# Kernel optimization log

Hardware: AMD Instinct MI355X
Metric: run time of the kernel (lower is better)

Reference implementation:

```python
import jax, jax.numpy as jnp
import numpy as np
from jax import lax

EPS = 1e-5

def conv2d(x, w, b, pad):
    # x: [N,C,H,W], w: [O,I,kh,kw]
    y = lax.conv_general_dilated(x, w, (1, 1), [(pad, pad), (pad, pad)],
                                 dimension_numbers=('NCHW', 'OIHW', 'NCHW'))
    return y + b[None, :, None, None]

def bn(x, g, b, axes, pshape):
    # training-mode batch norm (biased variance), matching torch BatchNorm2d in train()
    m = jnp.mean(x, axes, keepdims=True)
    v = jnp.var(x, axes, keepdims=True)
    return (x - m) * lax.rsqrt(v + EPS) * g.reshape(pshape) + b.reshape(pshape)

def maxpool2(x):
    return lax.reduce_window(x, -jnp.inf, lax.max, (1, 1, 2, 2), (1, 1, 2, 2), 'VALID')

def setup_inputs() -> dict:
    key = jax.random.key(0)
    ks = jax.random.split(key, 8)
    B, S, C, H, W = 8, 20, 16, 96, 96
    inp = {
        'anchor': jax.random.normal(ks[0], (B, C, H, W), jnp.float32),
        'support': jax.random.normal(ks[1], (B, S, C, H, W), jnp.float32),
        'cw': jax.random.normal(ks[2], (16, 16, 3, 3), jnp.float32) * 0.1,
        'cb': jnp.zeros((16,), jnp.float32),
        'cg': jnp.ones((16,), jnp.float32),
        'cbt': jnp.zeros((16,), jnp.float32),
        'pw': jax.random.normal(ks[3], (16, 32, 1, 1), jnp.float32) * 0.1,
        'pb': jnp.zeros((16,), jnp.float32),
        'pg': jnp.ones((16,), jnp.float32),
        'pbt': jnp.zeros((16,), jnp.float32),
        'jw': jax.random.normal(ks[4], (16, 16, 3, 3), jnp.float32) * 0.1,
        'jb': jnp.zeros((16,), jnp.float32),
        'jg': jnp.ones((16,), jnp.float32),
        'jbt': jnp.zeros((16,), jnp.float32),
        'rw': jax.random.normal(ks[5], (16, 16, 3, 3), jnp.float32) * 0.1,
        'rb': jnp.zeros((16,), jnp.float32),
        'rg': jnp.ones((16,), jnp.float32),
        'rbt': jnp.zeros((16,), jnp.float32),
    }
    return inp

def reference(anchor, support, cw, cb, cg, cbt, pw, pb, pg, pbt,
              jw, jb, jg, jbt, rw, rb, rg, rbt):
    B, S, C, H, W = support.shape
    # reshaper(anchor): conv3x3 -> BN -> ReLU -> maxpool2   (BN stats over B,H,W)
    ax = maxpool2(jax.nn.relu(bn(conv2d(anchor, rw, rb, 1), rg, rbt, (0, 2, 3), (1, -1, 1, 1))))
    # reshaper(support flattened): BN stats pooled over B*S,H,W (matches torch view(-1,...))
    sflat = support.reshape(B * S, C, H, W)
    sr = maxpool2(jax.nn.relu(bn(conv2d(sflat, rw, rb, 1), rg, rbt, (0, 2, 3), (1, -1, 1, 1))))
    sr = sr.reshape(B, S, C, H // 2, W // 2)
    # concentrator(support flattened)
    sx = jax.nn.relu(bn(conv2d(sflat, cw, cb, 1), cg, cbt, (0, 2, 3), (1, -1, 1, 1)))
    sx = sx.reshape(B, S, C, H, W)
    # leave-one-out sum via total-sum trick (O(S) instead of O(S^2))
    loo = sx.sum(axis=1, keepdims=True) - sx              # [B,S,C,H,W]
    cat = jnp.concatenate([support, loo], axis=2)         # [B,S,2C,H,W]
    pe = conv2d(cat.reshape(B * S, 2 * C, H, W), pw, pb, 0).reshape(B, S, C, H, W)
    # torch loop applies perm_equi per-i: BN stats over (B,H,W) for each support index
    pe = jax.nn.relu(bn(pe, pg, pbt, (0, 3, 4), (1, 1, -1, 1, 1)))
    deep = pe.mean(axis=1)                                # [B,C,H,W]
    # projector: conv3x3 -> BN -> softmax over channels -> maxpool2
    proj = maxpool2(jax.nn.softmax(bn(conv2d(deep, jw, jb, 1), jg, jbt, (0, 2, 3), (1, -1, 1, 1)), axis=1))
    anchor_out = ax * proj                                # [B,C,H/2,W/2]
    support_out = sr * proj[:, None]                      # [B,S,C,H/2,W/2]
    return anchor_out, support_out
```

## Files before the change

### kernel.cpp

```cpp
#include <hip/hip_runtime.h>
#include <stdint.h>

#define EPS_BN 1e-5f

typedef __attribute__((ext_vector_type(8))) short short8;
typedef __attribute__((ext_vector_type(4))) float floatx4;

__device__ __forceinline__ unsigned short f2bf(float f) {
    unsigned u = __builtin_bit_cast(unsigned, f);
    u += 0x7fffu + ((u >> 16) & 1u);
    return (unsigned short)(u >> 16);
}
__device__ __forceinline__ float bf2f(unsigned short h) {
    unsigned u = ((unsigned)h) << 16;
    return __builtin_bit_cast(float, u);
}
__device__ __forceinline__ void unpack8(uint4 q, float* v) {
    v[0] = bf2f((unsigned short)q.x); v[1] = bf2f((unsigned short)(q.x >> 16));
    v[2] = bf2f((unsigned short)q.y); v[3] = bf2f((unsigned short)(q.y >> 16));
    v[4] = bf2f((unsigned short)q.z); v[5] = bf2f((unsigned short)(q.z >> 16));
    v[6] = bf2f((unsigned short)q.w); v[7] = bf2f((unsigned short)(q.w >> 16));
}
__device__ __forceinline__ uint4 pack8(const float* v) {
    uint4 q;
    q.x = (unsigned)f2bf(v[0]) | ((unsigned)f2bf(v[1]) << 16);
    q.y = (unsigned)f2bf(v[2]) | ((unsigned)f2bf(v[3]) << 16);
    q.z = (unsigned)f2bf(v[4]) | ((unsigned)f2bf(v[5]) << 16);
    q.w = (unsigned)f2bf(v[6]) | ((unsigned)f2bf(v[7]) << 16);
    return q;
}

__device__ __forceinline__ void async_copy16(const unsigned short* g, unsigned short* l) {
    __builtin_amdgcn_global_load_lds(
        (const __attribute__((address_space(1))) unsigned int*)(const void*)g,
        (__attribute__((address_space(3))) unsigned int*)(void*)l,
        16, 0, 0);
}

__device__ __forceinline__ void bn_coef(const float* st, int n, int c, float invN,
                                        const float* gg, const float* bb,
                                        float* scl, float* shf) {
    const float mean = st[c] * invN;
    const float var = st[n + c] * invN - mean * mean;
    const float sc = gg[c & 15] * rsqrtf(var + EPS_BN);
    scl[c] = sc;
    shf[c] = bb[c & 15] - mean * sc;
}

__global__ __launch_bounds__(256)
void pack_kernel(const float* __restrict__ support, const float* __restrict__ anchor,
                 unsigned short* __restrict__ spad, unsigned short* __restrict__ apad,
                 const float* __restrict__ rw, const float* __restrict__ cw,
                 const float* __restrict__ jw, unsigned short* __restrict__ frag,
                 float* __restrict__ stats)
{
    const int tid = threadIdx.x;
    if (blockIdx.x >= 6303) {
        const int bx = blockIdx.x - 6303;
        if (bx == 4) {
            #pragma unroll
            for (int k = 0; k < 3; ++k) stats[k * 256 + tid] = 0.f;
            return;
        }
        const int idx = bx * 256 + tid;
        if (idx >= 960) return;
        const int combo = idx >> 6, lane = idx & 63;
        const int cv = combo / 5, j = combo - cv * 5;
        const float* w = (cv == 0) ? rw : (cv == 1) ? cw : jw;
        const int o = lane & 15, g = lane >> 4;
        unsigned short e8[8];
        #pragma unroll
        for (int e = 0; e < 8; ++e) {
            const int k = j * 32 + g * 8 + e;
            unsigned short val = 0;
            if (k < 144) {
                const int t = k >> 4, i = k & 15;
                const int kh = t / 3, kw = t - kh * 3;
                val = f2bf(w[((o * 16 + i) * 3 + kh) * 3 + kw]);
            }
            e8[e] = val;
        }
        *(uint4*)(frag + ((size_t)combo * 64 + lane) * 8) =
            make_uint4((unsigned)e8[0] | ((unsigned)e8[1] << 16), (unsigned)e8[2] | ((unsigned)e8[3] << 16),
                       (unsigned)e8[4] | ((unsigned)e8[5] << 16), (unsigned)e8[6] | ((unsigned)e8[7] << 16));
        return;
    }
    const int idx = blockIdx.x * 256 + tid;
    if (idx >= 168 * 9604) return;
    const int img = idx / 9604;
    const int rem = idx - img * 9604;
    const int pr = rem / 98, pc = rem - pr * 98;
    const int gh = pr - 1, gw = pc - 1;
    const bool ok = (gh >= 0) & (gh < 96) & (gw >= 0) & (gw < 96);
    const float* src = (img < 160) ? (support + (size_t)img * 147456)
                                   : (anchor + (size_t)(img - 160) * 147456);
    unsigned short* dst = (img < 160) ? (spad + (size_t)img * 9604 * 16)
                                      : (apad + (size_t)(img - 160) * 9604 * 16);
    const int gbase = gh * 96 + gw;
    unsigned pk[8];
    #pragma unroll
    for (int c = 0; c < 8; ++c) {
        const float v0 = ok ? src[(2 * c) * 9216 + gbase] : 0.f;
        const float v1 = ok ? src[(2 * c + 1) * 9216 + gbase] : 0.f;
        pk[c] = (unsigned)f2bf(v0) | ((unsigned)f2bf(v1) << 16);
    }
    const int sw = (pc >> 2) & 1;
    unsigned short* p = dst + (size_t)rem * 16;
    *(uint4*)(p + (sw << 3)) = make_uint4(pk[0], pk[1], pk[2], pk[3]);
    *(uint4*)(p + ((sw ^ 1) << 3)) = make_uint4(pk[4], pk[5], pk[6], pk[7]);
}

template<bool POOLA>
__device__ __forceinline__ void conv_tile(
    unsigned short* lds, float* red,
    const unsigned short* __restrict__ imgin,
    const unsigned short* __restrict__ fragA, const float* __restrict__ bA,
    const unsigned short* __restrict__ fragB, const float* __restrict__ bB,
    unsigned short* __restrict__ outAimg, unsigned short* __restrict__ outBimg,
    float* __restrict__ statsA, float* __restrict__ statsB,
    const int r0b, const bool two)
{
    const int tid = threadIdx.x;
    const int lane = tid & 63;
    const int wv = tid >> 6;

    const unsigned short* gsrc = imgin + (size_t)(r0b * 8 * 98) * 16;
    #pragma unroll
    for (int k = 0; k < 8; ++k) {
        const int chunk = k * 256 + tid;
        if (chunk < 1960)
            async_copy16(gsrc + (size_t)chunk * 8, lds + (k * 256 + wv * 64) * 8);
    }

    const int n = lane & 15, g = lane >> 4;
    short8 fA[5], fB[5];
    #pragma unroll
    for (int j = 0; j < 5; ++j) {
        fA[j] = *(const short8*)(fragA + ((size_t)j * 64 + lane) * 8);
        if (two) fB[j] = *(const short8*)(fragB + ((size_t)j * 64 + lane) * 8);
    }
    const float4 bA4 = *(const float4*)(bA + 4 * g);
    float4 bB4 = make_float4(0.f, 0.f, 0.f, 0.f);
    if (two) bB4 = *(const float4*)(bB + 4 * g);
    const float biasA[4] = {bA4.x, bA4.y, bA4.z, bA4.w};
    const float biasB[4] = {bB4.x, bB4.y, bB4.z, bB4.w};

    __syncthreads();

    float s1A[4] = {0.f, 0.f, 0.f, 0.f}, s2A[4] = {0.f, 0.f, 0.f, 0.f};
    float s1B[4] = {0.f, 0.f, 0.f, 0.f}, s2B[4] = {0.f, 0.f, 0.f, 0.f};

    for (int cg = 0; cg < 6; ++cg) {
        float pA[2][4], pB[2][4];
        #pragma unroll
        for (int tr = 0; tr < 2; ++tr) {
            const int lr = 2 * wv + tr;
            floatx4 aA = {0.f, 0.f, 0.f, 0.f};
            floatx4 aB = {0.f, 0.f, 0.f, 0.f};
            #pragma unroll
            for (int j = 0; j < 5; ++j) {
                const int t = (j < 4) ? (2 * j + (g >> 1)) : 8;
                const int kh = t / 3, kw = t - kh * 3;
                const int ldscol = cg * 16 + n + kw;
                const int half = (g & 1) ^ ((ldscol >> 2) & 1);
                const short8 a = *(const short8*)&lds[((lr + kh) * 98 + ldscol) * 16 + (half << 3)];
                aA = __builtin_amdgcn_mfma_f32_16x16x32_bf16(fA[j], a, aA, 0, 0, 0);
                if (two) aB = __builtin_amdgcn_mfma_f32_16x16x32_bf16(fB[j], a, aB, 0, 0, 0);
            }
            #pragma unroll
            for (int r = 0; r < 4; ++r) {
                const float vA = aA[r] + biasA[r];
                pA[tr][r] = vA; s1A[r] += vA; s2A[r] += vA * vA;
                if (two) {
                    const float vB = aB[r] + biasB[r];
                    pB[tr][r] = vB; s1B[r] += vB; s2B[r] += vB * vB;
                }
            }
            const int grow = r0b * 8 + lr;
            const size_t pixbase = ((size_t)(grow * 96 + cg * 16 + n)) * 16 + 4 * g;
            if (two)
                *(uint2*)(outBimg + pixbase) =
                    make_uint2((unsigned)f2bf(pB[tr][0]) | ((unsigned)f2bf(pB[tr][1]) << 16),
                               (unsigned)f2bf(pB[tr][2]) | ((unsigned)f2bf(pB[tr][3]) << 16));
            if (!POOLA)
                *(uint2*)(outAimg + pixbase) =
                    make_uint2((unsigned)f2bf(pA[tr][0]) | ((unsigned)f2bf(pA[tr][1]) << 16),
                               (unsigned)f2bf(pA[tr][2]) | ((unsigned)f2bf(pA[tr][3]) << 16));
        }
        if (POOLA) {
            float pm[4];
            #pragma unroll
            for (int r = 0; r < 4; ++r) {
                pm[r] = fmaxf(pA[0][r], pA[1][r]);
                pm[r] = fmaxf(pm[r], __shfl_xor(pm[r], 1));
            }
            if (!(n & 1)) {
                const int orow = r0b * 4 + wv;
                const size_t ob = ((size_t)(orow * 48 + cg * 8 + (n >> 1))) * 16 + 4 * g;
                *(uint2*)(outAimg + ob) =
                    make_uint2((unsigned)f2bf(pm[0]) | ((unsigned)f2bf(pm[1]) << 16),
                               (unsigned)f2bf(pm[2]) | ((unsigned)f2bf(pm[3]) << 16));
            }
        }
    }

    #pragma unroll
    for (int r = 0; r < 4; ++r) {
        #pragma unroll
        for (int d = 1; d < 16; d <<= 1) {
            s1A[r] += __shfl_xor(s1A[r], d); s2A[r] += __shfl_xor(s2A[r], d);
            if (two) { s1B[r] += __shfl_xor(s1B[r], d); s2B[r] += __shfl_xor(s2B[r], d); }
        }
    }
    if (n == 0) {
        #pragma unroll
        for (int r = 0; r < 4; ++r) {
            red[(wv * 4 + 0) * 16 + g * 4 + r] = s1A[r];
            red[(wv * 4 + 1) * 16 + g * 4 + r] = s2A[r];
            if (two) {
                red[(wv * 4 + 2) * 16 + g * 4 + r] = s1B[r];
                red[(wv * 4 + 3) * 16 + g * 4 + r] = s2B[r];
            }
        }
    }
    __syncthreads();
    if (tid < (two ? 64 : 32)) {
        const int st = tid >> 4, oc = tid & 15;
        const float v = red[(0 * 4 + st) * 16 + oc] + red[(1 * 4 + st) * 16 + oc] +
                        red[(2 * 4 + st) * 16 + oc] + red[(3 * 4 + st) * 16 + oc];
        float* dst = (st < 2) ? statsA : statsB;
        atomicAdd(&dst[(st & 1) * 16 + oc], v);
    }
}

__global__ __launch_bounds__(256)
void conv_main_kernel(const unsigned short* __restrict__ spad, const unsigned short* __restrict__ apad,
                      const unsigned short* __restrict__ fragR, const float* __restrict__ rb,
                      const unsigned short* __restrict__ fragC, const float* __restrict__ cb,
                      unsigned short* __restrict__ srp, unsigned short* __restrict__ sxpe,
                      unsigned short* __restrict__ axp,
                      float* __restrict__ statsSr, float* __restrict__ statsSx,
                      float* __restrict__ statsAx)
{
    __shared__ __align__(16) unsigned short lds[10 * 98 * 16];
    __shared__ float red[4 * 4 * 16];
    const bool two = blockIdx.x < 1920;
    const int bid = two ? blockIdx.x : blockIdx.x - 1920;
    const int img = bid / 12;
    const int r0b = bid - img * 12;
    const unsigned short* in = (two ? spad : apad) + (size_t)img * 9604 * 16;
    unsigned short* outA = (two ? srp : axp) + (size_t)img * 2304 * 16;
    unsigned short* outB = sxpe + (size_t)img * 9216 * 16;
    conv_tile<true>(lds, red, in, fragR, rb, fragC, cb, outA, outB,
                    two ? statsSr : statsAx, statsSx, r0b, two);
}

__global__ __launch_bounds__(256)
void conv_j_kernel(const unsigned short* __restrict__ deeppad,
                   const unsigned short* __restrict__ fragJ, const float* __restrict__ jb,
                   unsigned short* __restrict__ pre_j, float* __restrict__ statsJ)
{
    __shared__ __align__(16) unsigned short lds[10 * 98 * 16];
    __shared__ float red[4 * 4 * 16];
    const int img = blockIdx.x / 12;
    const int r0b = blockIdx.x - img * 12;
    conv_tile<false>(lds, red, deeppad + (size_t)img * 9604 * 16, fragJ, jb, nullptr, nullptr,
                     pre_j + (size_t)img * 9216 * 16, nullptr, statsJ, nullptr, r0b, false);
}

__global__ __launch_bounds__(256)
void sxsum_kernel(const unsigned short* __restrict__ sx, const float* __restrict__ statsSx,
                  const float* __restrict__ cgm, const float* __restrict__ cbt,
                  float* __restrict__ out, unsigned short* __restrict__ deeppad)
{
    __shared__ float scl[16], shf[16];
    __shared__ float part[3][64][17];
    const int tid = threadIdx.x;
    if (blockIdx.x < 13) {
        const int idx = blockIdx.x * 256 + tid;
        if (idx < 8 * 388) {
            const int img = idx / 388;
            const int h = idx - img * 388;
            int pr, pc;
            if (h < 98)       { pr = 0;           pc = h; }
            else if (h < 196) { pr = 97;          pc = h - 98; }
            else if (h < 292) { pr = h - 196 + 1; pc = 0; }
            else              { pr = h - 292 + 1; pc = 97; }
            unsigned short* p = deeppad + ((size_t)img * 9604 + pr * 98 + pc) * 16;
            *(uint4*)p = make_uint4(0, 0, 0, 0);
            *(uint4*)(p + 8) = make_uint4(0, 0, 0, 0);
        }
    }
    if (tid < 16) bn_coef(statsSx, 16, tid, 1.f / 1474560.f, cgm, cbt, scl, shf);
    const int b = blockIdx.x / 144;
    const int chunk = blockIdx.x - b * 144;
    const int px = tid & 63, sg = tid >> 6;
    const int pix = chunk * 64 + px;
    __syncthreads();
    float acc[16];
    #pragma unroll
    for (int c = 0; c < 16; ++c) acc[c] = 0.f;
    const unsigned short* p = sx + ((size_t)(b * 20 + sg * 5) * 9216 + pix) * 16;
    #pragma unroll
    for (int s = 0; s < 5; ++s) {
        float v[16];
        unpack8(*(const uint4*)p, v);
        unpack8(*(const uint4*)(p + 8), v + 8);
        #pragma unroll
        for (int c = 0; c < 16; ++c) acc[c] += fmaxf(v[c] * scl[c] + shf[c], 0.f);
        p += 9216 * 16;
    }
    if (sg > 0) {
        #pragma unroll
        for (int c = 0; c < 16; ++c) part[sg - 1][px][c] = acc[c];
    }
    __syncthreads();
    if (sg == 0) {
        #pragma unroll
        for (int c = 0; c < 16; ++c) acc[c] += part[0][px][c] + part[1][px][c] + part[2][px][c];
        float* o = out + ((size_t)b * 9216 + pix) * 16;
        #pragma unroll
        for (int q = 0; q < 4; ++q)
            *(float4*)(o + 4 * q) = make_float4(acc[4 * q], acc[4 * q + 1], acc[4 * q + 2], acc[4 * q + 3]);
    }
}

__global__ __launch_bounds__(256)
void pe_kernel(const unsigned short* __restrict__ spad, unsigned short* __restrict__ sxpe,
               const float* __restrict__ sxsum, const float* __restrict__ statsSx,
               const float* __restrict__ cgm, const float* __restrict__ cbt,
               const float* __restrict__ pw, const float* __restrict__ pb,
               float* __restrict__ statsPe)
{
    __shared__ float sscl[16], sshf[16];
    __shared__ float red[4][2][16];
    const int tid = threadIdx.x;
    if (tid < 16) bn_coef(statsSx, 16, tid, 1.f / 1474560.f, cgm, cbt, sscl, sshf);
    const int lane = tid & 63, wv = tid >> 6;
    const int p = lane & 15, g = lane >> 4;
    const int img = blockIdx.x / 9;
    const int chunk = blockIdx.x - img * 9;
    const int b = img / 20, s = img - b * 20;
    const int c0 = (g & 1) * 8;

    short8 fw;
    {
        const float4 wa = *(const float4*)(pw + p * 32 + g * 8);
        const float4 wb = *(const float4*)(pw + p * 32 + g * 8 + 4);
        fw[0] = (short)f2bf(wa.x); fw[1] = (short)f2bf(wa.y);
        fw[2] = (short)f2bf(wa.z); fw[3] = (short)f2bf(wa.w);
        fw[4] = (short)f2bf(wb.x); fw[5] = (short)f2bf(wb.y);
        fw[6] = (short)f2bf(wb.z); fw[7] = (short)f2bf(wb.w);
    }
    const float4 b4 = *(const float4*)(pb + 4 * g);
    const float bias[4] = {b4.x, b4.y, b4.z, b4.w};
    __syncthreads();
    float scl[8], shf[8];
    #pragma unroll
    for (int e = 0; e < 8; ++e) { scl[e] = sscl[c0 + e]; shf[e] = sshf[c0 + e]; }

    const unsigned short* imgspad = spad + (size_t)img * 9604 * 16;
    unsigned short* imgsx = sxpe + (size_t)img * 9216 * 16;
    const float* bsum = sxsum + (size_t)b * 9216 * 16;

    float s1[4] = {0.f, 0.f, 0.f, 0.f}, s2[4] = {0.f, 0.f, 0.f, 0.f};

    for (int it = 0; it < 16; ++it) {
        const int pix = chunk * 1024 + it * 64 + wv * 16 + p;
        short8 bf;
        if (g < 2) {
            const int row = pix / 96, col = pix - row * 96;
            const int sw = ((col + 1) >> 2) & 1;
            bf = *(const short8*)(imgspad + ((row + 1) * 98 + col + 1) * 16 + (((g ^ sw) & 1) << 3));
        } else {
            float xv[8];
            unpack8(*(const uint4*)(imgsx + (size_t)pix * 16 + c0), xv);
            const float* sm = bsum + (size_t)pix * 16 + c0;
            const float4 sma = *(const float4*)sm;
            const float4 smb = *(const float4*)(sm + 4);
            const float smv[8] = {sma.x, sma.y, sma.z, sma.w, smb.x, smb.y, smb.z, smb.w};
            #pragma unroll
            for (int e = 0; e < 8; ++e) {
                const float loo = smv[e] - fmaxf(xv[e] * scl[e] + shf[e], 0.f);
                bf[e] = (short)f2bf(loo);
            }
        }
        floatx4 acc = {0.f, 0.f, 0.f, 0.f};
        acc = __builtin_amdgcn_mfma_f32_16x16x32_bf16(fw, bf, acc, 0, 0, 0);
        const float v0 = acc[0] + bias[0], v1 = acc[1] + bias[1];
        const float v2 = acc[2] + bias[2], v3 = acc[3] + bias[3];
        s1[0] += v0; s1[1] += v1; s1[2] += v2; s1[3] += v3;
        s2[0] += v0 * v0; s2[1] += v1 * v1; s2[2] += v2 * v2; s2[3] += v3 * v3;
        *(uint2*)(imgsx + (size_t)pix * 16 + 4 * g) =
            make_uint2((unsigned)f2bf(v0) | ((unsigned)f2bf(v1) << 16),
                       (unsigned)f2bf(v2) | ((unsigned)f2bf(v3) << 16));
    }

    #pragma unroll
    for (int r = 0; r < 4; ++r) {
        #pragma unroll
        for (int d = 1; d < 16; d <<= 1) {
            s1[r] += __shfl_xor(s1[r], d);
            s2[r] += __shfl_xor(s2[r], d);
        }
    }
    if (p == 0) {
        #pragma unroll
        for (int r = 0; r < 4; ++r) { red[wv][0][g * 4 + r] = s1[r]; red[wv][1][g * 4 + r] = s2[r]; }
    }
    __syncthreads();
    if (tid < 32) {
        const int st = tid >> 4, c = tid & 15;
        const float v = red[0][st][c] + red[1][st][c] + red[2][st][c] + red[3][st][c];
        atomicAdd(&statsPe[st * 320 + s * 16 + c], v);
    }
}

__global__ __launch_bounds__(256)
void deep_kernel(const unsigned short* __restrict__ pe, const float* __restrict__ statsPe,
                 const float* __restrict__ pg, const float* __restrict__ pbt,
                 unsigned short* __restrict__ deeppad)
{
    __shared__ float scl[320], shf[320];
    __shared__ float part[3][64][17];
    const int tid = threadIdx.x;
    for (int i = tid; i < 320; i += 256)
        bn_coef(statsPe, 320, i, 1.f / 73728.f, pg, pbt, scl, shf);
    const int b = blockIdx.x / 144;
    const int chunk = blockIdx.x - b * 144;
    const int px = tid & 63, sg = tid >> 6;
    const int pix = chunk * 64 + px;
    __syncthreads();
    float acc[16];
    #pragma unroll
    for (int c = 0; c < 16; ++c) acc[c] = 0.f;
    const unsigned short* p = pe + ((size_t)(b * 20 + sg * 5) * 9216 + pix) * 16;
    #pragma unroll
    for (int s = 0; s < 5; ++s) {
        const int si = sg * 5 + s;
        float v[16];
        unpack8(*(const uint4*)p, v);
        unpack8(*(const uint4*)(p + 8), v + 8);
        #pragma unroll
        for (int c = 0; c < 16; ++c) acc[c] += fmaxf(v[c] * scl[si * 16 + c] + shf[si * 16 + c], 0.f);
        p += 9216 * 16;
    }
    if (sg > 0) {
        #pragma unroll
        for (int c = 0; c < 16; ++c) part[sg - 1][px][c] = acc[c];
    }
    __syncthreads();
    if (sg == 0) {
        #pragma unroll
        for (int c = 0; c < 16; ++c)
            acc[c] = (acc[c] + part[0][px][c] + part[1][px][c] + part[2][px][c]) * 0.05f;
        const int row = pix / 96, col = pix - row * 96;
        const int sw = ((col + 1) >> 2) & 1;
        unsigned short* d = deeppad + ((size_t)b * 9604 + (row + 1) * 98 + col + 1) * 16;
        *(uint4*)(d + (sw << 3)) = pack8(acc);
        *(uint4*)(d + ((sw ^ 1) << 3)) = pack8(acc + 8);
    }
}

__global__ __launch_bounds__(256)
void proj_kernel(const unsigned short* __restrict__ pj, const float* __restrict__ statsJ,
                 const float* __restrict__ jg, const float* __restrict__ jbt,
                 float* __restrict__ proj)
{
    __shared__ float scl[16], shf[16];
    const int tid = threadIdx.x;
    if (tid < 16) bn_coef(statsJ, 16, tid, 1.f / 73728.f, jg, jbt, scl, shf);
    const int b = blockIdx.x / 9;
    const int opix = (blockIdx.x - b * 9) * 256 + tid;
    __syncthreads();
    const int oi = opix / 48, oj = opix - oi * 48;
    float mx[16];
    #pragma unroll
    for (int c = 0; c < 16; ++c) mx[c] = 0.f;
    #pragma unroll
    for (int dy = 0; dy < 2; ++dy) {
        const unsigned short* q = pj + ((size_t)b * 9216 + (2 * oi + dy) * 96 + 2 * oj) * 16;
        #pragma unroll
        for (int dx = 0; dx < 2; ++dx) {
            float v[16]; float mval = -1e30f;
            unpack8(*(const uint4*)(q + dx * 16), v);
            unpack8(*(const uint4*)(q + dx * 16 + 8), v + 8);
            #pragma unroll
            for (int c = 0; c < 16; ++c) { v[c] = v[c] * scl[c] + shf[c]; mval = fmaxf(mval, v[c]); }
            float ssum = 0.f;
            #pragma unroll
            for (int c = 0; c < 16; ++c) { v[c] = __expf(v[c] - mval); ssum += v[c]; }
            const float inv = 1.f / ssum;
            #pragma unroll
            for (int c = 0; c < 16; ++c) mx[c] = fmaxf(mx[c], v[c] * inv);
        }
    }
    float* o = proj + ((size_t)b * 2304 + opix) * 16;
    #pragma unroll
    for (int q2 = 0; q2 < 4; ++q2)
        *(float4*)(o + 4 * q2) = make_float4(mx[4 * q2], mx[4 * q2 + 1], mx[4 * q2 + 2], mx[4 * q2 + 3]);
}

__global__ __launch_bounds__(256)
void out_kernel(const unsigned short* __restrict__ srp, const unsigned short* __restrict__ axp,
                const float* __restrict__ statsSr, const float* __restrict__ statsAx,
                const float* __restrict__ rg, const float* __restrict__ rbt,
                const float* __restrict__ proj, float* __restrict__ outS,
                float* __restrict__ outA)
{
    __shared__ float scl[16], shf[16];
    const int tid = threadIdx.x;
    const bool sup = blockIdx.x < 1440;
    if (tid < 16) {
        if (sup) bn_coef(statsSr, 16, tid, 1.f / 1474560.f, rg, rbt, scl, shf);
        else     bn_coef(statsAx, 16, tid, 1.f / 73728.f, rg, rbt, scl, shf);
    }
    const int bid = sup ? blockIdx.x : blockIdx.x - 1440;
    const int bs = bid / 9;
    const int opix = (bid - bs * 9) * 256 + tid;
    const int b = sup ? bs / 20 : bs;
    __syncthreads();
    const unsigned short* p = (sup ? srp : axp) + ((size_t)bs * 2304 + opix) * 16;
    float v[16];
    unpack8(*(const uint4*)p, v);
    unpack8(*(const uint4*)(p + 8), v + 8);
    const float* pr = proj + ((size_t)b * 2304 + opix) * 16;
    float* o = sup ? outS : outA;
    #pragma unroll
    for (int c = 0; c < 16; ++c)
        o[((size_t)bs * 16 + c) * 2304 + opix] = fmaxf(v[c] * scl[c] + shf[c], 0.f) * pr[c];
}

extern "C" void kernel_launch(void* const* d_in, const int* in_sizes, int n_in,
                              void* d_out, int out_size, void* d_ws, size_t ws_size,
                              hipStream_t stream)
{
    const float* anchor  = (const float*)d_in[0];
    const float* support = (const float*)d_in[1];
    const float* cw  = (const float*)d_in[2];
    const float* cb  = (const float*)d_in[3];
    const float* cgm = (const float*)d_in[4];
    const float* cbt = (const float*)d_in[5];
    const float* pw  = (const float*)d_in[6];
    const float* pb  = (const float*)d_in[7];
    const float* pg  = (const float*)d_in[8];
    const float* pbt = (const float*)d_in[9];
    const float* jw  = (const float*)d_in[10];
    const float* jb  = (const float*)d_in[11];
    const float* jg  = (const float*)d_in[12];
    const float* jbt = (const float*)d_in[13];
    const float* rw  = (const float*)d_in[14];
    const float* rb  = (const float*)d_in[15];
    const float* rg  = (const float*)d_in[16];
    const float* rbt = (const float*)d_in[17];
    float* out = (float*)d_out;

    char* ws = (char*)d_ws;
    unsigned short* spad    = (unsigned short*)ws;
    unsigned short* pre_j   = (unsigned short*)(ws + 2458624);
    float*          proj    = (float*)(ws + 4817920);
    unsigned short* apad    = (unsigned short*)(ws + 49172480);
    unsigned short* deeppad = apad;
    unsigned short* sxpe    = (unsigned short*)(ws + 51631104);
    unsigned short* srp     = (unsigned short*)(ws + 98817024);
    unsigned short* axp     = (unsigned short*)(ws + 110613504);
    float*          sxsum   = (float*)(ws + 111203328);
    unsigned short* frag    = (unsigned short*)(ws + 115921920);
    float*          stats   = (float*)(ws + 115937280);

    unsigned short* fragR = frag;
    unsigned short* fragC = frag + 5 * 64 * 8;
    unsigned short* fragJ = frag + 10 * 64 * 8;
    float* statsAx = stats,      *statsSr = stats + 32, *statsSx = stats + 64;
    float* statsPe = stats + 96, *statsJ  = stats + 736;

    pack_kernel<<<6308, 256, 0, stream>>>(support, anchor, spad, apad, rw, cw, jw, frag, stats);
    conv_main_kernel<<<2016, 256, 0, stream>>>(spad, apad, fragR, rb, fragC, cb,
                                               srp, sxpe, axp, statsSr, statsSx, statsAx);
    sxsum_kernel<<<1152, 256, 0, stream>>>(sxpe, statsSx, cgm, cbt, sxsum, deeppad);
    pe_kernel<<<1440, 256, 0, stream>>>(spad, sxpe, sxsum, statsSx, cgm, cbt, pw, pb, statsPe);
    deep_kernel<<<1152, 256, 0, stream>>>(sxpe, statsPe, pg, pbt, deeppad);
    conv_j_kernel<<<96, 256, 0, stream>>>(deeppad, fragJ, jb, pre_j, statsJ);
    proj_kernel<<<72, 256, 0, stream>>>(pre_j, statsJ, jg, jbt, proj);
    out_kernel<<<1512, 256, 0, stream>>>(srp, axp, statsSr, statsAx, rg, rbt, proj,
                                         out + 294912, out);
}
```

Baseline: 144.8 us.

## Fuse support-sum and permutation-equivariant conv kernels via LDS-staged sx tile

Merges sxsum_kernel and pe_kernel into one kernel. Each block loads a 64-pixel chunk of sx for all 20 support images, keeps the raw values in LDS, reduces the sum there, and then computes the leave-one-out MFMA 1x1 conv without writing or re-reading the fp32 sxsum buffer or re-reading sx from global memory. This removes one launch plus the sxsum traffic. The cost is a large LDS footprint (~51KB plus psum), which lowers occupancy. It also adds a different butterfly-shuffle reduction for the stats atomics, with more atomics per block.

```diff
diff --git a/kernel.cpp b/kernel.cpp
--- a/kernel.cpp
+++ b/kernel.cpp
@@ -269,12 +269,16 @@
 }
 
 __global__ __launch_bounds__(256)
-void sxsum_kernel(const unsigned short* __restrict__ sx, const float* __restrict__ statsSx,
-                  const float* __restrict__ cgm, const float* __restrict__ cbt,
-                  float* __restrict__ out, unsigned short* __restrict__ deeppad)
-{
-    __shared__ float scl[16], shf[16];
-    __shared__ float part[3][64][17];
+void pe_fused_kernel(const unsigned short* __restrict__ spad, unsigned short* __restrict__ sxpe,
+                     const float* __restrict__ statsSx,
+                     const float* __restrict__ cgm, const float* __restrict__ cbt,
+                     const float* __restrict__ pw, const float* __restrict__ pb,
+                     float* __restrict__ statsPe, unsigned short* __restrict__ deeppad)
+{
+    __shared__ __align__(16) unsigned short sxl[20 * 64 * 20];
+    __shared__ float psum[2][64][17];
+    __shared__ float sscl[16], sshf[16];
+
     const int tid = threadIdx.x;
     if (blockIdx.x < 13) {
         const int idx = blockIdx.x * 256 + tid;
@@ -291,58 +295,57 @@
             *(uint4*)(p + 8) = make_uint4(0, 0, 0, 0);
         }
     }
-    if (tid < 16) bn_coef(statsSx, 16, tid, 1.f / 1474560.f, cgm, cbt, scl, shf);
+    if (tid < 16) bn_coef(statsSx, 16, tid, 1.f / 1474560.f, cgm, cbt, sscl, sshf);
     const int b = blockIdx.x / 144;
     const int chunk = blockIdx.x - b * 144;
-    const int px = tid & 63, sg = tid >> 6;
-    const int pix = chunk * 64 + px;
-    __syncthreads();
+    const int pix0 = chunk * 64;
+    __syncthreads();
+
+    const int px = tid & 63;
+    const int sgrp = tid >> 6;
+    const int swz = (px >> 4) & 1;
     float acc[16];
     #pragma unroll
     for (int c = 0; c < 16; ++c) acc[c] = 0.f;
-    const unsigned short* p = sx + ((size_t)(b * 20 + sg * 5) * 9216 + pix) * 16;
-    #pragma unroll
-    for (int s = 0; s < 5; ++s) {
-        float v[16];
-        unpack8(*(const uint4*)p, v);
-        unpack8(*(const uint4*)(p + 8), v + 8);
-        #pragma unroll
-        for (int c = 0; c < 16; ++c) acc[c] += fmaxf(v[c] * scl[c] + shf[c], 0.f);
-        p += 9216 * 16;
-    }
-    if (sg > 0) {
-        #pragma unroll
-        for (int c = 0; c < 16; ++c) part[sg - 1][px][c] = acc[c];
-    }
-    __syncthreads();
-    if (sg == 0) {
-        #pragma unroll
-        for (int c = 0; c < 16; ++c) acc[c] += part[0][px][c] + part[1][px][c] + part[2][px][c];
-        float* o = out + ((size_t)b * 9216 + pix) * 16;
-        #pragma unroll
-        for (int q = 0; q < 4; ++q)
-            *(float4*)(o + 4 * q) = make_float4(acc[4 * q], acc[4 * q + 1], acc[4 * q + 2], acc[4 * q + 3]);
-    }
-}
-
-__global__ __launch_bounds__(256)
-void pe_kernel(const unsigned short* __restrict__ spad, unsigned short* __restrict__ sxpe,
-               const float* __restrict__ sxsum, const float* __restrict__ statsSx,
-               const float* __restrict__ cgm, const float* __restrict__ cbt,
-               const float* __restrict__ pw, const float* __restrict__ pb,
-               float* __restrict__ statsPe)
-{
-    __shared__ float sscl[16], sshf[16];
-    __shared__ float red[4][2][16];
-    const int tid = threadIdx.x;
-    if (tid < 16) bn_coef(statsSx, 16, tid, 1.f / 1474560.f, cgm, cbt, sscl, sshf);
+    {
+        const unsigned short* srcp = sxpe + ((size_t)(b * 20 + sgrp * 5) * 9216 + pix0 + px) * 16;
+        for (int s = 0; s < 5; ++s) {
+            const uint4 lo = *(const uint4*)srcp;
+            const uint4 hi = *(const uint4*)(srcp + 8);
+            float v[16];
+            unpack8(lo, v); unpack8(hi, v + 8);
+            #pragma unroll
+            for (int c = 0; c < 16; ++c) acc[c] += fmaxf(v[c] * sscl[c] + sshf[c], 0.f);
+            unsigned short* dst = sxl + ((sgrp * 5 + s) * 64 + px) * 20;
+            unsigned short* d0 = dst + (swz << 3);
+            unsigned short* d1 = dst + ((swz ^ 1) << 3);
+            *(uint2*)d0 = make_uint2(lo.x, lo.y);
+            *(uint2*)(d0 + 4) = make_uint2(lo.z, lo.w);
+            *(uint2*)d1 = make_uint2(hi.x, hi.y);
+            *(uint2*)(d1 + 4) = make_uint2(hi.z, hi.w);
+            srcp += (size_t)9216 * 16;
+        }
+    }
+    if (sgrp < 2) {
+        #pragma unroll
+        for (int c = 0; c < 16; ++c) psum[sgrp][px][c] = acc[c];
+    }
+    __syncthreads();
+    if (sgrp >= 2) {
+        #pragma unroll
+        for (int c = 0; c < 16; ++c) psum[sgrp - 2][px][c] += acc[c];
+    }
+    __syncthreads();
+    {
+        const int cq = tid >> 6, px2 = tid & 63;
+        #pragma unroll
+        for (int i = 0; i < 4; ++i) psum[0][px2][cq * 4 + i] += psum[1][px2][cq * 4 + i];
+    }
+    __syncthreads();
+
     const int lane = tid & 63, wv = tid >> 6;
     const int p = lane & 15, g = lane >> 4;
-    const int img = blockIdx.x / 9;
-    const int chunk = blockIdx.x - img * 9;
-    const int b = img / 20, s = img - b * 20;
     const int c0 = (g & 1) * 8;
-
     short8 fw;
     {
         const float4 wa = *(const float4*)(pw + p * 32 + g * 8);
@@ -354,65 +357,72 @@
     }
     const float4 b4 = *(const float4*)(pb + 4 * g);
     const float bias[4] = {b4.x, b4.y, b4.z, b4.w};
-    __syncthreads();
-    float scl[8], shf[8];
-    #pragma unroll
-    for (int e = 0; e < 8; ++e) { scl[e] = sscl[c0 + e]; shf[e] = sshf[c0 + e]; }
-
-    const unsigned short* imgspad = spad + (size_t)img * 9604 * 16;
-    unsigned short* imgsx = sxpe + (size_t)img * 9216 * 16;
-    const float* bsum = sxsum + (size_t)b * 9216 * 16;
-
-    float s1[4] = {0.f, 0.f, 0.f, 0.f}, s2[4] = {0.f, 0.f, 0.f, 0.f};
-
-    for (int it = 0; it < 16; ++it) {
-        const int pix = chunk * 1024 + it * 64 + wv * 16 + p;
-        short8 bf;
-        if (g < 2) {
-            const int row = pix / 96, col = pix - row * 96;
-            const int sw = ((col + 1) >> 2) & 1;
-            bf = *(const short8*)(imgspad + ((row + 1) * 98 + col + 1) * 16 + (((g ^ sw) & 1) << 3));
-        } else {
-            float xv[8];
-            unpack8(*(const uint4*)(imgsx + (size_t)pix * 16 + c0), xv);
-            const float* sm = bsum + (size_t)pix * 16 + c0;
-            const float4 sma = *(const float4*)sm;
-            const float4 smb = *(const float4*)(sm + 4);
-            const float smv[8] = {sma.x, sma.y, sma.z, sma.w, smb.x, smb.y, smb.z, smb.w};
-            #pragma unroll
-            for (int e = 0; e < 8; ++e) {
-                const float loo = smv[e] - fmaxf(xv[e] * scl[e] + shf[e], 0.f);
-                bf[e] = (short)f2bf(loo);
-            }
-        }
-        floatx4 acc = {0.f, 0.f, 0.f, 0.f};
-        acc = __builtin_amdgcn_mfma_f32_16x16x32_bf16(fw, bf, acc, 0, 0, 0);
-        const float v0 = acc[0] + bias[0], v1 = acc[1] + bias[1];
-        const float v2 = acc[2] + bias[2], v3 = acc[3] + bias[3];
-        s1[0] += v0; s1[1] += v1; s1[2] += v2; s1[3] += v3;
-        s2[0] += v0 * v0; s2[1] += v1 * v1; s2[2] += v2 * v2; s2[3] += v3 * v3;
-        *(uint2*)(imgsx + (size_t)pix * 16 + 4 * g) =
-            make_uint2((unsigned)f2bf(v0) | ((unsigned)f2bf(v1) << 16),
-                       (unsigned)f2bf(v2) | ((unsigned)f2bf(v3) << 16));
-    }
-
-    #pragma unroll
-    for (int r = 0; r < 4; ++r) {
-        #pragma unroll
-        for (int d = 1; d < 16; d <<= 1) {
-            s1[r] += __shfl_xor(s1[r], d);
-            s2[r] += __shfl_xor(s2[r], d);
-        }
-    }
-    if (p == 0) {
-        #pragma unroll
-        for (int r = 0; r < 4; ++r) { red[wv][0][g * 4 + r] = s1[r]; red[wv][1][g * 4 + r] = s2[r]; }
-    }
-    __syncthreads();
-    if (tid < 32) {
-        const int st = tid >> 4, c = tid & 15;
-        const float v = red[0][st][c] + red[1][st][c] + red[2][st][c] + red[3][st][c];
-        atomicAdd(&statsPe[st * 320 + s * 16 + c], v);
+
+    for (int sw = 0; sw < 5; ++sw) {
+        const int s = wv + sw * 4;
+        const int img = b * 20 + s;
+        const unsigned short* imgspad = spad + (size_t)img * 9604 * 16;
+        unsigned short* imgsx = sxpe + ((size_t)img * 9216 + pix0) * 16;
+        float s1[4] = {0.f, 0.f, 0.f, 0.f}, s2[4] = {0.f, 0.f, 0.f, 0.f};
+        for (int tile = 0; tile < 4; ++tile) {
+            const int pixl = tile * 16 + p;
+            short8 bf;
+            if (g < 2) {
+                const int pix = pix0 + pixl;
+                const int row = pix / 96, col = pix - row * 96;
+                const int sw2 = ((col + 1) >> 2) & 1;
+                bf = *(const short8*)(imgspad + ((row + 1) * 98 + col + 1) * 16 + (((g ^ sw2) & 1) << 3));
+            } else {
+                const int hh = (g & 1) ^ ((pixl >> 4) & 1);
+                const unsigned short* srcl = sxl + (s * 64 + pixl) * 20 + (hh << 3);
+                const uint2 qa = *(const uint2*)srcl;
+                const uint2 qb = *(const uint2*)(srcl + 4);
+                float xv[8];
+                unpack8(make_uint4(qa.x, qa.y, qb.x, qb.y), xv);
+                #pragma unroll
+                for (int e = 0; e < 8; ++e) {
+                    const float relu = fmaxf(xv[e] * sscl[c0 + e] + sshf[c0 + e], 0.f);
+                    bf[e] = (short)f2bf(psum[0][pixl][c0 + e] - relu);
+                }
+            }
+            floatx4 acc2 = {0.f, 0.f, 0.f, 0.f};
+            acc2 = __builtin_amdgcn_mfma_f32_16x16x32_bf16(fw, bf, acc2, 0, 0, 0);
+            const float v0 = acc2[0] + bias[0], v1 = acc2[1] + bias[1];
+            const float v2 = acc2[2] + bias[2], v3 = acc2[3] + bias[3];
+            s1[0] += v0; s1[1] += v1; s1[2] += v2; s1[3] += v3;
+            s2[0] += v0 * v0; s2[1] += v1 * v1; s2[2] += v2 * v2; s2[3] += v3 * v3;
+            *(uint2*)(imgsx + (size_t)pixl * 16 + 4 * g) =
+                make_uint2((unsigned)f2bf(v0) | ((unsigned)f2bf(v1) << 16),
+                           (unsigned)f2bf(v2) | ((unsigned)f2bf(v3) << 16));
+        }
+        float v8[8] = {s1[0], s1[1], s1[2], s1[3], s2[0], s2[1], s2[2], s2[3]};
+        {
+            const bool hi = (lane & 1) != 0;
+            float t[4], u[4];
+            #pragma unroll
+            for (int k = 0; k < 4; ++k) { t[k] = hi ? v8[k + 4] : v8[k]; u[k] = hi ? v8[k] : v8[k + 4]; }
+            #pragma unroll
+            for (int k = 0; k < 4; ++k) v8[k] = t[k] + __shfl_xor(u[k], 1);
+        }
+        {
+            const bool hi = (lane & 2) != 0;
+            float t[2], u[2];
+            #pragma unroll
+            for (int k = 0; k < 2; ++k) { t[k] = hi ? v8[k + 2] : v8[k]; u[k] = hi ? v8[k] : v8[k + 2]; }
+            #pragma unroll
+            for (int k = 0; k < 2; ++k) v8[k] = t[k] + __shfl_xor(u[k], 2);
+        }
+        {
+            const bool hi = (lane & 4) != 0;
+            const float t = hi ? v8[1] : v8[0], u = hi ? v8[0] : v8[1];
+            v8[0] = t + __shfl_xor(u, 4);
+        }
+        v8[0] += __shfl_xor(v8[0], 8);
+        if (p < 8) {
+            const int stat = p & 1;
+            const int r = ((p >> 1) & 1) * 2 + ((p >> 2) & 1);
+            atomicAdd(&statsPe[stat * 320 + s * 16 + g * 4 + r], v8[0]);
+        }
     }
 }
 
@@ -564,7 +574,6 @@
     unsigned short* sxpe    = (unsigned short*)(ws + 51631104);
     unsigned short* srp     = (unsigned short*)(ws + 98817024);
     unsigned short* axp     = (unsigned short*)(ws + 110613504);
-    float*          sxsum   = (float*)(ws + 111203328);
     unsigned short* frag    = (unsigned short*)(ws + 115921920);
     float*          stats   = (float*)(ws + 115937280);
 
@@ -577,8 +586,8 @@
     pack_kernel<<<6308, 256, 0, stream>>>(support, anchor, spad, apad, rw, cw, jw, frag, stats);
     conv_main_kernel<<<2016, 256, 0, stream>>>(spad, apad, fragR, rb, fragC, cb,
                                                srp, sxpe, axp, statsSr, statsSx, statsAx);
-    sxsum_kernel<<<1152, 256, 0, stream>>>(sxpe, statsSx, cgm, cbt, sxsum, deeppad);
-    pe_kernel<<<1440, 256, 0, stream>>>(spad, sxpe, sxsum, statsSx, cgm, cbt, pw, pb, statsPe);
+    pe_fused_kernel<<<1152, 256, 0, stream>>>(spad, sxpe, statsSx, cgm, cbt, pw, pb,
+                                              statsPe, deeppad);
     deep_kernel<<<1152, 256, 0, stream>>>(sxpe, statsPe, pg, pbt, deeppad);
     conv_j_kernel<<<96, 256, 0, stream>>>(deeppad, fragJ, jb, pre_j, statsJ);
     proj_kernel<<<72, 256, 0, stream>>>(pre_j, statsJ, jg, jbt, proj);
```

After: 162.2 us. +12.0%, slower.
